# Performance work log

Measured on AMD Instinct MI355X. Metric: run time of the kernel, lower is better.

## Reference

```python
import jax, jax.numpy as jnp
import numpy as np

EPS = 1e-3  # sscp_conv_group_norm_eps


def setup_inputs() -> dict:
    key = jax.random.key(0)
    k1, k2, k3 = jax.random.split(key, 3)
    audio_encodings = jax.random.normal(k1, (4, 1, 4096, 128), dtype=jnp.float32)
    # Conv2d(in=1, out=128, kernel=(3,3), stride=(2,2), bias=False), OIHW layout
    conv_w = jax.random.normal(k2, (128, 1, 3, 3), dtype=jnp.float32) * 0.1
    # AudioCumulativeGroupNorm per-channel scale (init ones; randomize slightly)
    norm_scale = jnp.ones((128,), dtype=jnp.float32) + 0.01 * jax.random.normal(k3, (128,), dtype=jnp.float32)
    return {"audio_encodings": audio_encodings, "conv_w": conv_w, "norm_scale": norm_scale}


def reference(audio_encodings, conv_w, norm_scale):
    # manual_padding = (0, 1, 1, 1) in torch F.pad order (W_left, W_right, H_top, H_bottom)
    x = jnp.pad(audio_encodings, ((0, 0), (0, 0), (1, 1), (0, 1)))
    # Conv2d stride (2,2), no padding, no bias
    y = jax.lax.conv_general_dilated(
        x, conv_w, window_strides=(2, 2), padding='VALID',
        dimension_numbers=('NCHW', 'OIHW', 'NCHW'))  # [B, C, T, F]
    # permute to [B, T, F, C] and normalize cumulatively over T (mask=None)
    h = jnp.transpose(y, (0, 2, 3, 1)).astype(jnp.float32)
    B, T, F, C = h.shape
    # cumulative count of elements per group at each t: (t+1) * F * C
    cnt = (jnp.arange(1, T + 1, dtype=jnp.float32) * (F * C)).reshape(1, T, 1, 1)
    cum_sum = jnp.cumsum(jnp.sum(h, axis=(2, 3), keepdims=True), axis=1)  # [B,T,1,1]
    cum_mean = cum_sum / cnt
    sq = jnp.sum((h - cum_mean) ** 2, axis=(2, 3), keepdims=True)
    cum_var = jnp.cumsum(sq, axis=1) / cnt
    normed = (h - cum_mean) * jax.lax.rsqrt(cum_var + EPS) * norm_scale  # scale per channel (last dim)
    out = jnp.transpose(normed, (0, 3, 1, 2))  # back to [B, C, T, F]
    return jax.nn.relu(out)
```

## Files before the change

### kernel.cpp

```cpp
#include <hip/hip_runtime.h>

#define X_H 4096
#define X_W 128
#define BATCH 4
#define CH 128
#define TT_OUT 2048
#define FF 64
#define EPS_GN 1e-3f

#define WSUM_OFF 0
#define M_OFF 16
#define S1_OFF 128
#define SS_OFF (S1_OFF + BATCH*TT_OUT)
#define MU_OFF (SS_OFF + BATCH*TT_OUT)
#define ISTD_OFF (MU_OFF + BATCH*TT_OUT)

__global__ void prep_kernel(const float* __restrict__ w, float* __restrict__ ws) {
    int tid = threadIdx.x;
    if (tid < 81) {
        int j = tid / 9, k = tid % 9;
        float acc = 0.f;
        for (int c = 0; c < CH; ++c) acc = fmaf(w[c*9 + j], w[c*9 + k], acc);
        ws[M_OFF + tid] = acc;
    } else if (tid < 90) {
        int k = tid - 81;
        float acc = 0.f;
        for (int c = 0; c < CH; ++c) acc += w[c*9 + k];
        ws[WSUM_OFF + k] = acc;
    }
}

__global__ __launch_bounds__(256) void stats_kernel(const float* __restrict__ x,
                                                    float* __restrict__ ws) {
    int tid = threadIdx.x;
    int wid = blockIdx.x * 4 + (tid >> 6);
    int lane = tid & 63;
    int t = wid & (TT_OUT - 1);
    int b = wid >> 11;
    int f = lane;
    const float* xb = x + (size_t)b * (X_H * X_W);
    float xv[9];
    int r0 = 2*t - 1;
#pragma unroll
    for (int kh = 0; kh < 3; ++kh) {
        int r = r0 + kh;
        bool rok = (r >= 0) && (r < X_H);
#pragma unroll
        for (int kw = 0; kw < 3; ++kw) {
            int cidx = 2*f + kw;
            xv[kh*3+kw] = (rok && cidx < X_W) ? xb[(size_t)r * X_W + cidx] : 0.f;
        }
    }
    float s1 = 0.f, ss = 0.f;
#pragma unroll
    for (int k = 0; k < 9; ++k) s1 = fmaf(ws[WSUM_OFF + k], xv[k], s1);
#pragma unroll
    for (int j = 0; j < 9; ++j) {
        float tj = 0.f;
#pragma unroll
        for (int k = 0; k < 9; ++k) tj = fmaf(ws[M_OFF + j*9 + k], xv[k], tj);
        ss = fmaf(xv[j], tj, ss);
    }
#pragma unroll
    for (int off = 32; off > 0; off >>= 1) {
        s1 += __shfl_xor(s1, off);
        ss += __shfl_xor(ss, off);
    }
    if (lane == 0) {
        ws[S1_OFF + wid] = s1;
        ws[SS_OFF + wid] = ss;
    }
}

__global__ __launch_bounds__(256) void scan_kernel(float* __restrict__ ws) {
    int b = blockIdx.x;
    int tid = threadIdx.x;
    int lane = tid & 63;
    int wv = tid >> 6;
    const float* S1 = ws + S1_OFF + b*TT_OUT;
    const float* SS = ws + SS_OFF + b*TT_OUT;
    float* MU = ws + MU_OFF + b*TT_OUT;
    float* ISTD = ws + ISTD_OFF + b*TT_OUT;
    __shared__ double wsum_lds[4];

    double s1loc[8], v[8];
    double tot = 0.0;
#pragma unroll
    for (int i = 0; i < 8; ++i) { s1loc[i] = (double)S1[tid*8+i]; tot += s1loc[i]; v[i] = tot; }
    double incl = tot;
#pragma unroll
    for (int off = 1; off < 64; off <<= 1) {
        double n = __shfl_up(incl, off);
        if (lane >= off) incl += n;
    }
    if (lane == 63) wsum_lds[wv] = incl;
    __syncthreads();
    double woff = 0.0;
    for (int w2 = 0; w2 < wv; ++w2) woff += wsum_lds[w2];
    double prefix = woff + incl - tot;

    double muloc[8], sqv[8], v2[8];
    double tot2 = 0.0;
#pragma unroll
    for (int i = 0; i < 8; ++i) {
        int t = tid*8 + i;
        double cs = prefix + v[i];
        double cnt = (double)(t+1) * 8192.0;
        double mu = cs / cnt;
        double sq = (double)SS[t] - 2.0*mu*s1loc[i] + 8192.0*mu*mu;
        muloc[i] = mu;
        tot2 += sq; v2[i] = tot2;
    }
    double incl2 = tot2;
#pragma unroll
    for (int off = 1; off < 64; off <<= 1) {
        double n = __shfl_up(incl2, off);
        if (lane >= off) incl2 += n;
    }
    __syncthreads();
    if (lane == 63) wsum_lds[wv] = incl2;
    __syncthreads();
    double woff2 = 0.0;
    for (int w2 = 0; w2 < wv; ++w2) woff2 += wsum_lds[w2];
    double prefix2 = woff2 + incl2 - tot2;
#pragma unroll
    for (int i = 0; i < 8; ++i) {
        int t = tid*8 + i;
        double cnt = (double)(t+1) * 8192.0;
        double var = (prefix2 + v2[i]) / cnt;
        MU[t] = (float)muloc[i];
        ISTD[t] = rsqrtf((float)var + EPS_GN);
    }
}

#define T_TILE 16
#define CG 16
__global__ __launch_bounds__(256) void out_kernel(const float* __restrict__ x,
        const float* __restrict__ w, const float* __restrict__ scale,
        const float* __restrict__ ws, float* __restrict__ out) {
    __shared__ float wl[CG][9];
    __shared__ float sl[CG];
    int tid = threadIdx.x;
    int b = blockIdx.z;
    int c0 = blockIdx.y * CG;
    int t0 = blockIdx.x * T_TILE;
    if (tid < CG*9) wl[tid/9][tid%9] = w[c0*9 + tid];
    if (tid < CG) sl[tid] = scale[c0 + tid];
    __syncthreads();
    int f = tid & 63;
    int trow = tid >> 6;
    const float* xb = x + (size_t)b * (X_H * X_W);
    const float* MU = ws + MU_OFF + b*TT_OUT;
    const float* ISTD = ws + ISTD_OFF + b*TT_OUT;
#pragma unroll
    for (int it = 0; it < T_TILE/4; ++it) {
        int t = t0 + it*4 + trow;
        float mu = MU[t];
        float istd = ISTD[t];
        float xv[9];
        int r0 = 2*t - 1;
#pragma unroll
        for (int kh = 0; kh < 3; ++kh) {
            int r = r0 + kh;
            bool rok = (r >= 0) && (r < X_H);
#pragma unroll
            for (int kw = 0; kw < 3; ++kw) {
                int cidx = 2*f + kw;
                xv[kh*3+kw] = (rok && cidx < X_W) ? xb[(size_t)r * X_W + cidx] : 0.f;
            }
        }
        float* ob = out + (((size_t)(b*CH + c0) * TT_OUT + t) * FF + f);
#pragma unroll
        for (int c = 0; c < CG; ++c) {
            float h = 0.f;
#pragma unroll
            for (int k = 0; k < 9; ++k) h = fmaf(wl[c][k], xv[k], h);
            float a = istd * sl[c];
            float val = fmaf(h, a, -mu * a);
            val = fmaxf(val, 0.f);
            ob[(size_t)c * (TT_OUT * FF)] = val;
        }
    }
}

extern "C" void kernel_launch(void* const* d_in, const int* in_sizes, int n_in,
                              void* d_out, int out_size, void* d_ws, size_t ws_size,
                              hipStream_t stream) {
    const float* x     = (const float*)d_in[0];
    const float* w     = (const float*)d_in[1];
    const float* scale = (const float*)d_in[2];
    float* out = (float*)d_out;
    float* ws  = (float*)d_ws;

    prep_kernel<<<1, 128, 0, stream>>>(w, ws);
    stats_kernel<<<(BATCH*TT_OUT)/4, 256, 0, stream>>>(x, ws);
    scan_kernel<<<BATCH, 256, 0, stream>>>(ws);
    out_kernel<<<dim3(TT_OUT/T_TILE, CH/CG, BATCH), 256, 0, stream>>>(x, w, scale, ws, out);
}
```

Baseline: 65.27 us.

## Vectorize loads/stores with 4 outputs per thread, fuse prep into stats kernel

Result: faster. 62.66 us (-4.0%).

```diff
diff --git a/kernel.cpp b/kernel.cpp
--- a/kernel.cpp
+++ b/kernel.cpp
@@ -8,67 +8,84 @@
 #define FF 64
 #define EPS_GN 1e-3f
 
-#define WSUM_OFF 0
-#define M_OFF 16
-#define S1_OFF 128
-#define SS_OFF (S1_OFF + BATCH*TT_OUT)
-#define MU_OFF (SS_OFF + BATCH*TT_OUT)
-#define ISTD_OFF (MU_OFF + BATCH*TT_OUT)
-
-__global__ void prep_kernel(const float* __restrict__ w, float* __restrict__ ws) {
+typedef float f4 __attribute__((ext_vector_type(4)));
+typedef float f2 __attribute__((ext_vector_type(2)));
+
+#define S1_OFF 0
+#define SS_OFF (BATCH*TT_OUT)
+#define MI_OFF (2*BATCH*TT_OUT)
+
+__global__ __launch_bounds__(256) void stats_kernel(const float* __restrict__ x,
+                                                    const float* __restrict__ w,
+                                                    float* __restrict__ ws) {
+    __shared__ float Ml[81];
+    __shared__ float Wl[9];
     int tid = threadIdx.x;
     if (tid < 81) {
         int j = tid / 9, k = tid % 9;
         float acc = 0.f;
         for (int c = 0; c < CH; ++c) acc = fmaf(w[c*9 + j], w[c*9 + k], acc);
-        ws[M_OFF + tid] = acc;
+        Ml[tid] = acc;
     } else if (tid < 90) {
         int k = tid - 81;
         float acc = 0.f;
         for (int c = 0; c < CH; ++c) acc += w[c*9 + k];
-        ws[WSUM_OFF + k] = acc;
-    }
-}
-
-__global__ __launch_bounds__(256) void stats_kernel(const float* __restrict__ x,
-                                                    float* __restrict__ ws) {
-    int tid = threadIdx.x;
-    int wid = blockIdx.x * 4 + (tid >> 6);
-    int lane = tid & 63;
-    int t = wid & (TT_OUT - 1);
-    int b = wid >> 11;
-    int f = lane;
+        Wl[k] = acc;
+    }
+    __syncthreads();
+
+    int fq = tid & 15;
+    int tr = tid >> 4;
+    int gt = blockIdx.x * 16 + tr;
+    int t = gt & (TT_OUT - 1);
+    int b = gt >> 11;
     const float* xb = x + (size_t)b * (X_H * X_W);
-    float xv[9];
+
+    float xr[3][9];
     int r0 = 2*t - 1;
 #pragma unroll
     for (int kh = 0; kh < 3; ++kh) {
         int r = r0 + kh;
-        bool rok = (r >= 0) && (r < X_H);
-#pragma unroll
-        for (int kw = 0; kw < 3; ++kw) {
-            int cidx = 2*f + kw;
-            xv[kh*3+kw] = (rok && cidx < X_W) ? xb[(size_t)r * X_W + cidx] : 0.f;
-        }
-    }
+        if (r >= 0 && r < X_H) {
+            const float* rp = xb + (size_t)r * X_W + 8*fq;
+            f4 v0 = *(const f4*)rp;
+            f4 v1 = *(const f4*)(rp + 4);
+            xr[kh][0]=v0.x; xr[kh][1]=v0.y; xr[kh][2]=v0.z; xr[kh][3]=v0.w;
+            xr[kh][4]=v1.x; xr[kh][5]=v1.y; xr[kh][6]=v1.z; xr[kh][7]=v1.w;
+            xr[kh][8] = (fq == 15) ? 0.f : rp[8];
+        } else {
+#pragma unroll
+            for (int k = 0; k < 9; ++k) xr[kh][k] = 0.f;
+        }
+    }
+
     float s1 = 0.f, ss = 0.f;
 #pragma unroll
-    for (int k = 0; k < 9; ++k) s1 = fmaf(ws[WSUM_OFF + k], xv[k], s1);
-#pragma unroll
-    for (int j = 0; j < 9; ++j) {
-        float tj = 0.f;
-#pragma unroll
-        for (int k = 0; k < 9; ++k) tj = fmaf(ws[M_OFF + j*9 + k], xv[k], tj);
-        ss = fmaf(xv[j], tj, ss);
-    }
-#pragma unroll
-    for (int off = 32; off > 0; off >>= 1) {
+    for (int jf = 0; jf < 4; ++jf) {
+        float tv[9];
+#pragma unroll
+        for (int kh = 0; kh < 3; ++kh)
+#pragma unroll
+            for (int kw = 0; kw < 3; ++kw)
+                tv[kh*3+kw] = xr[kh][2*jf + kw];
+#pragma unroll
+        for (int k = 0; k < 9; ++k) s1 = fmaf(Wl[k], tv[k], s1);
+#pragma unroll
+        for (int j = 0; j < 9; ++j) {
+            float tj = 0.f;
+#pragma unroll
+            for (int k = 0; k < 9; ++k) tj = fmaf(Ml[j*9+k], tv[k], tj);
+            ss = fmaf(tv[j], tj, ss);
+        }
+    }
+#pragma unroll
+    for (int off = 1; off < 16; off <<= 1) {
         s1 += __shfl_xor(s1, off);
         ss += __shfl_xor(ss, off);
     }
-    if (lane == 0) {
-        ws[S1_OFF + wid] = s1;
-        ws[SS_OFF + wid] = ss;
+    if (fq == 0) {
+        ws[S1_OFF + gt] = s1;
+        ws[SS_OFF + gt] = ss;
     }
 }
 
@@ -79,8 +96,7 @@
     int wv = tid >> 6;
     const float* S1 = ws + S1_OFF + b*TT_OUT;
     const float* SS = ws + SS_OFF + b*TT_OUT;
-    float* MU = ws + MU_OFF + b*TT_OUT;
-    float* ISTD = ws + ISTD_OFF + b*TT_OUT;
+    f2* MI = (f2*)(ws + MI_OFF) + b*TT_OUT;
     __shared__ double wsum_lds[4];
 
     double s1loc[8], v[8];
@@ -99,7 +115,7 @@
     for (int w2 = 0; w2 < wv; ++w2) woff += wsum_lds[w2];
     double prefix = woff + incl - tot;
 
-    double muloc[8], sqv[8], v2[8];
+    double muloc[8], v2[8];
     double tot2 = 0.0;
 #pragma unroll
     for (int i = 0; i < 8; ++i) {
@@ -128,8 +144,10 @@
         int t = tid*8 + i;
         double cnt = (double)(t+1) * 8192.0;
         double var = (prefix2 + v2[i]) / cnt;
-        MU[t] = (float)muloc[i];
-        ISTD[t] = rsqrtf((float)var + EPS_GN);
+        f2 mi;
+        mi.x = (float)muloc[i];
+        mi.y = rsqrtf((float)var + EPS_GN);
+        MI[t] = mi;
     }
 }
 
@@ -147,39 +165,50 @@
     if (tid < CG*9) wl[tid/9][tid%9] = w[c0*9 + tid];
     if (tid < CG) sl[tid] = scale[c0 + tid];
     __syncthreads();
-    int f = tid & 63;
-    int trow = tid >> 6;
+
+    int fq = tid & 15;
+    int tr = tid >> 4;
+    int t = t0 + tr;
     const float* xb = x + (size_t)b * (X_H * X_W);
-    const float* MU = ws + MU_OFF + b*TT_OUT;
-    const float* ISTD = ws + ISTD_OFF + b*TT_OUT;
-#pragma unroll
-    for (int it = 0; it < T_TILE/4; ++it) {
-        int t = t0 + it*4 + trow;
-        float mu = MU[t];
-        float istd = ISTD[t];
-        float xv[9];
-        int r0 = 2*t - 1;
-#pragma unroll
-        for (int kh = 0; kh < 3; ++kh) {
-            int r = r0 + kh;
-            bool rok = (r >= 0) && (r < X_H);
-#pragma unroll
-            for (int kw = 0; kw < 3; ++kw) {
-                int cidx = 2*f + kw;
-                xv[kh*3+kw] = (rok && cidx < X_W) ? xb[(size_t)r * X_W + cidx] : 0.f;
-            }
-        }
-        float* ob = out + (((size_t)(b*CH + c0) * TT_OUT + t) * FF + f);
-#pragma unroll
-        for (int c = 0; c < CG; ++c) {
+    f2 mi = ((const f2*)(ws + MI_OFF))[b*TT_OUT + t];
+    float mu = mi.x, istd = mi.y;
+
+    float xr[3][9];
+    int r0 = 2*t - 1;
+#pragma unroll
+    for (int kh = 0; kh < 3; ++kh) {
+        int r = r0 + kh;
+        if (r >= 0 && r < X_H) {
+            const float* rp = xb + (size_t)r * X_W + 8*fq;
+            f4 v0 = *(const f4*)rp;
+            f4 v1 = *(const f4*)(rp + 4);
+            xr[kh][0]=v0.x; xr[kh][1]=v0.y; xr[kh][2]=v0.z; xr[kh][3]=v0.w;
+            xr[kh][4]=v1.x; xr[kh][5]=v1.y; xr[kh][6]=v1.z; xr[kh][7]=v1.w;
+            xr[kh][8] = (fq == 15) ? 0.f : rp[8];
+        } else {
+#pragma unroll
+            for (int k = 0; k < 9; ++k) xr[kh][k] = 0.f;
+        }
+    }
+
+    float* ob = out + (((size_t)(b*CH + c0) * TT_OUT + t) * FF + 4*fq);
+#pragma unroll
+    for (int c = 0; c < CG; ++c) {
+        float a  = istd * sl[c];
+        float nb = -mu * a;
+        f4 v;
+#pragma unroll
+        for (int jf = 0; jf < 4; ++jf) {
             float h = 0.f;
 #pragma unroll
-            for (int k = 0; k < 9; ++k) h = fmaf(wl[c][k], xv[k], h);
-            float a = istd * sl[c];
-            float val = fmaf(h, a, -mu * a);
-            val = fmaxf(val, 0.f);
-            ob[(size_t)c * (TT_OUT * FF)] = val;
-        }
+            for (int kh = 0; kh < 3; ++kh)
+#pragma unroll
+                for (int kw = 0; kw < 3; ++kw)
+                    h = fmaf(wl[c][kh*3+kw], xr[kh][2*jf + kw], h);
+            float val = fmaxf(fmaf(h, a, nb), 0.f);
+            v[jf] = val;
+        }
+        __builtin_nontemporal_store(v, (f4*)(ob + (size_t)c * (TT_OUT * FF)));
     }
 }
 
@@ -192,8 +221,7 @@
     float* out = (float*)d_out;
     float* ws  = (float*)d_ws;
 
-    prep_kernel<<<1, 128, 0, stream>>>(w, ws);
-    stats_kernel<<<(BATCH*TT_OUT)/4, 256, 0, stream>>>(x, ws);
+    stats_kernel<<<(BATCH*TT_OUT)/16, 256, 0, stream>>>(x, w, ws);
     scan_kernel<<<BATCH, 256, 0, stream>>>(ws);
     out_kernel<<<dim3(TT_OUT/T_TILE, CH/CG, BATCH), 256, 0, stream>>>(x, w, scale, ws, out);
 }
```
